# Kernel tuning notes

Measured on AMD Instinct MI355X. Metric: run time of the kernel, lower is better.

The kernel has to match this reference:

```python
import jax, jax.numpy as jnp
import numpy as np


def setup_inputs() -> dict:
    key = jax.random.key(0)
    ks = jax.random.split(key, 8)
    C, G, F = 500, 200, 500          # cells_oi, genes_oi, position bins (fragmentprob_size)
    N_GENES, N_CLUST = 1000, 10      # total genes, clusters
    NFRAG = 5_000_000
    bincounts = jax.random.randint(ks[0], (G, F), 0, 20).astype(jnp.float32)
    baseline_weight = jax.random.normal(ks[1], (N_GENES, F), jnp.float32) * 0.1
    differential_weight = jax.random.normal(ks[2], (N_CLUST, 1, 1), jnp.float32) * 0.01
    cluster_modifier = jax.random.normal(ks[3], (N_CLUST,), jnp.float32) * 0.01
    genes_oi = jax.random.randint(ks[4], (G,), 0, N_GENES)
    labels = jax.random.randint(ks[5], (C,), 0, N_CLUST)
    local_cellxgene_ix = jax.random.randint(ks[6], (NFRAG,), 0, C * G)
    binix = jax.random.randint(ks[7], (NFRAG,), 0, F)
    return dict(bincounts=bincounts, baseline_weight=baseline_weight,
                differential_weight=differential_weight, cluster_modifier=cluster_modifier,
                genes_oi=genes_oi, labels=labels,
                local_cellxgene_ix=local_cellxgene_ix, binix=binix)


def reference(bincounts, baseline_weight, differential_weight, cluster_modifier,
              genes_oi, labels, local_cellxgene_ix, binix):
    G, F = bincounts.shape
    C = labels.shape[0]
    # predictor2 is Identity, final_channels = n_hidden_dims = 1
    gene_embedding = bincounts[:, :, None]                     # [G, F, 1]
    baseline = baseline_weight[genes_oi]                       # [G, F]
    cell_embedding = differential_weight[labels][:, :, 0]      # [C, 1]
    # matmul([1,G,F,H], [C,1,H,1]).squeeze(-1) -> [C,G,F]
    u = (jnp.einsum('gfh,ch->cgf', gene_embedding, cell_embedding)
         + baseline[None]
         + cluster_modifier[labels][:, None, None])            # [C, G, F]
    # histogram of fragments into (cell x gene x bin)
    idx = local_cellxgene_ix * F + binix
    count = jnp.zeros(C * G * F, dtype=u.dtype).at[idx].add(1.0).reshape(C, G, F)
    # Poisson(rate=exp(u)).log_prob(count) = count*u - exp(u) - lgamma(count+1)
    logp = count * u - jnp.exp(u) - jax.lax.lgamma(count + 1.0)
    return logp.sum(-1)                                        # [C, G]
```

## Files before the change

### kernel.cpp

```cpp
#include <hip/hip_runtime.h>
#include <stdint.h>

#define C_   500
#define G_   200
#define F_   500
#define K_   10
#define CG_  (C_ * G_)
#define CGPB 125
#define NBUCK (CG_ / CGPB)
#define NVB  (NBUCK * 2)
#define RSTRIDE 504
#define WPR  (RSTRIDE / 8)
#define NCW2 (CGPB * WPR + 1)
#define TPB_P 1024
#define GRID_P 512
#define NBLK 512
#define TPB_B 512
#define CHUNK_MAX 10240
#define FPT2 (CHUNK_MAX / TPB_P / 2)
#define SLOT 40
#define OVF_CAP 16

__constant__ float LGF[16] = {
    0.0f, 0.0f, 0.69314718f, 1.79175947f, 3.17805383f, 4.78749174f,
    6.57925121f, 8.52516136f, 10.60460290f, 12.80182748f, 15.10441257f,
    17.50230785f, 19.98721450f, 22.55216385f, 25.19122118f, 27.89927138f
};

__global__ __launch_bounds__(TPB_P) void partition_kernel(
        const int* __restrict__ lci,
        const int* __restrict__ binix,
        const float* __restrict__ bc,
        const float* __restrict__ bw,
        const int* __restrict__ genes_oi,
        const float* __restrict__ dw,
        const float* __restrict__ cm,
        uint16_t* __restrict__ frag16,
        uint16_t* __restrict__ cnt16,
        uint32_t* __restrict__ ovfn,
        uint32_t* __restrict__ ovfe,
        float* __restrict__ u_tab,
        float* __restrict__ E,
        int NF, int chunk) {
    __shared__ uint32_t stage[CHUNK_MAX];
    __shared__ uint32_t hist[NVB];
    __shared__ uint32_t vstart[NVB];
    __shared__ uint32_t sstart[NBUCK];
    __shared__ float    psum[4];
    __shared__ uint32_t ovf_lds[OVF_CAP];
    __shared__ uint32_t oc;
    int tid = threadIdx.x;
    int blk = blockIdx.x;
    int copy = tid >> 9;
    int s0 = blk * chunk;
    int s1 = min(s0 + chunk, NF);
    int nloc = s1 - s0;

    for (int b = tid; b < NVB; b += TPB_P) hist[b] = 0;
    if (tid < 4) psum[tid] = 0.0f;
    if (tid == 0) oc = 0u;
    __syncthreads();

    {
        int p = blk * 4 + (tid >> 8);
        if (p < K_ * G_) {
            int sub = tid & 255;
            int k = p / G_;
            int g = p - k * G_;
            float dwk = dw[k];
            float cmk = cm[k];
            const float* bcg = bc + (size_t)g * F_;
            const float* bwg = bw + (size_t)genes_oi[g] * F_;
            float* urow = u_tab + (size_t)p * F_;
            float u0 = dwk * bcg[sub] + bwg[sub] + cmk;
            urow[sub] = u0;
            float s = __expf(u0);
            int f1 = sub + 256;
            if (f1 < F_) {
                float u1 = dwk * bcg[f1] + bwg[f1] + cmk;
                urow[f1] = u1;
                s += __expf(u1);
            }
#pragma unroll
            for (int off = 32; off > 0; off >>= 1) s += __shfl_down(s, off);
            if ((tid & 63) == 0) atomicAdd(&psum[tid >> 8], s);
        }
    }

    uint32_t my_pack[FPT2 * 2], my_rank[FPT2 * 2];
    const int2* lci2 = (const int2*)(lci + s0);
    const int2* bin2 = (const int2*)(binix + s0);
#pragma unroll
    for (int u = 0; u < FPT2; ++u) {
        int pi = u * TPB_P + tid;
        int e0 = pi * 2;
        my_pack[2 * u]     = 0xFFFFFFFFu;
        my_pack[2 * u + 1] = 0xFFFFFFFFu;
        if (e0 + 1 < nloc) {
            int2 cg2 = lci2[pi];
            int2 f2  = bin2[pi];
            uint32_t b0  = (uint32_t)cg2.x / CGPB;
            uint32_t lp0 = ((uint32_t)cg2.x - b0 * CGPB) * RSTRIDE + (uint32_t)f2.x;
            my_pack[2 * u] = (b0 << 16) | lp0;
            my_rank[2 * u] = atomicAdd(&hist[copy * NBUCK + b0], 1u);
            uint32_t b1  = (uint32_t)cg2.y / CGPB;
            uint32_t lp1 = ((uint32_t)cg2.y - b1 * CGPB) * RSTRIDE + (uint32_t)f2.y;
            my_pack[2 * u + 1] = (b1 << 16) | lp1;
            my_rank[2 * u + 1] = atomicAdd(&hist[copy * NBUCK + b1], 1u);
        } else if (e0 < nloc) {
            int cg = lci[s0 + e0];
            int f  = binix[s0 + e0];
            uint32_t b  = (uint32_t)cg / CGPB;
            uint32_t lp = ((uint32_t)cg - b * CGPB) * RSTRIDE + (uint32_t)f;
            my_pack[2 * u] = (b << 16) | lp;
            my_rank[2 * u] = atomicAdd(&hist[copy * NBUCK + b], 1u);
        }
    }
    __syncthreads();

    if (tid < 4) {
        int p = blk * 4 + tid;
        if (p < K_ * G_) E[p] = psum[tid];
    }
    if (tid < 64) {
        int lane = tid;
        uint32_t loc[13];
        uint32_t run = 0;
#pragma unroll
        for (int q = 0; q < 13; ++q) {
            int b = lane * 13 + q;
            uint32_t n = (b < NBUCK) ? (hist[b] + hist[NBUCK + b]) : 0u;
            loc[q] = run;
            run += n;
        }
        uint32_t v = run;
        for (int d = 1; d < 64; d <<= 1) {
            uint32_t t = __shfl_up(v, d);
            if (lane >= d) v += t;
        }
        uint32_t excl = v - run;
#pragma unroll
        for (int q = 0; q < 13; ++q) {
            int b = lane * 13 + q;
            if (b < NBUCK) {
                uint32_t st = excl + loc[q];
                sstart[b] = st;
                vstart[b]         = st;
                vstart[NBUCK + b] = st + hist[b];
            }
        }
    } else if (tid < 64 + NBUCK) {
        int b = tid - 64;
        uint32_t n = hist[b] + hist[NBUCK + b];
        cnt16[(size_t)blk * NBUCK + b] = (uint16_t)min(n, (uint32_t)SLOT);
    }
    __syncthreads();

#pragma unroll
    for (int u = 0; u < FPT2 * 2; ++u) {
        if (my_pack[u] != 0xFFFFFFFFu) {
            uint32_t bb = my_pack[u] >> 16;
            stage[vstart[copy * NBUCK + bb] + my_rank[u]] = my_pack[u];
        }
    }
    __syncthreads();

    for (int j = tid; j < nloc; j += TPB_P) {
        uint32_t v = stage[j];
        uint32_t b = v >> 16;
        uint32_t r = (uint32_t)j - sstart[b];
        if (r < SLOT)
            frag16[((size_t)b * NBLK + blk) * SLOT + r] = (uint16_t)v;
        else {
            uint32_t o = atomicAdd(&oc, 1u);
            if (o < OVF_CAP) ovf_lds[o] = v;
        }
    }
    __syncthreads();
    if (tid == 0) ovfn[blk] = min(oc, (uint32_t)OVF_CAP);
    if (tid < OVF_CAP && tid < oc) ovfe[blk * OVF_CAP + tid] = ovf_lds[tid];
}

__global__ __launch_bounds__(TPB_B) void bucket_kernel(
        const uint16_t* __restrict__ frag16,
        const uint16_t* __restrict__ cnt16,
        const uint32_t* __restrict__ ovfn,
        const uint32_t* __restrict__ ovfe,
        const float* __restrict__ u_tab,
        const float* __restrict__ E,
        const int* __restrict__ labels,
        float* __restrict__ out) {
    __shared__ uint32_t cnt[NCW2];
    __shared__ uint16_t cnts[NBLK];
    __shared__ int pairidx[CGPB];
    int b = blockIdx.x;
    int tid = threadIdx.x;

    uint4* c4 = (uint4*)cnt;
    for (int w = tid; w < NCW2 / 4; w += TPB_B) c4[w] = make_uint4(0u, 0u, 0u, 0u);
    if (tid < CGPB) {
        int cg = b * CGPB + tid;
        int c = cg / G_;
        int g = cg - c * G_;
        pairidx[tid] = labels[c] * G_ + g;
    }
    if (tid < NBLK) cnts[tid] = cnt16[(size_t)tid * NBUCK + b];
    __syncthreads();

    const uint4* fb4 = (const uint4*)(frag16 + (size_t)b * NBLK * SLOT);
    for (int i = tid; i < NBLK * 5; i += TPB_B) {
        uint32_t blk = (uint32_t)i / 5u;
        uint32_t q   = (uint32_t)i - blk * 5u;
        int n  = (int)cnts[blk];
        int j0 = (int)q * 8;
        if (j0 < n) {
            uint4 four = fb4[i];
            int m = n - j0;
            uint32_t w0 = four.x, w1 = four.y, w2 = four.z, w3 = four.w;
            uint32_t wq[4] = {w0, w1, w2, w3};
#pragma unroll
            for (int t = 0; t < 8; ++t) {
                if (t < m) {
                    uint32_t l = (wq[t >> 1] >> ((t & 1) * 16)) & 0xFFFFu;
                    atomicAdd(&cnt[l >> 3], 1u << ((l & 7u) * 4u));
                }
            }
        }
    }
    if (tid < NBLK) {
        uint32_t on = ovfn[tid];
        for (uint32_t q = 0; q < on; ++q) {
            uint32_t e = ovfe[tid * OVF_CAP + q];
            if ((e >> 16) == (uint32_t)b) {
                uint32_t l = e & 0xFFFFu;
                atomicAdd(&cnt[l >> 3], 1u << ((l & 7u) * 4u));
            }
        }
    }
    __syncthreads();

    int wave = tid >> 6, lane = tid & 63;
    for (int r = wave; r < CGPB; r += (TPB_B / 64)) {
        float s = 0.0f;
        if (lane < WPR) {
            uint32_t v = cnt[r * WPR + lane];
            if (v) {
                const float4* up = (const float4*)(u_tab + (size_t)pairidx[r] * F_ + 8 * lane);
                float4 ua = up[0];
                float4 ub = up[1];
                s += (float)( v        & 0xFu) * ua.x
                   + (float)((v >> 4)  & 0xFu) * ua.y
                   + (float)((v >> 8)  & 0xFu) * ua.z
                   + (float)((v >> 12) & 0xFu) * ua.w
                   + (float)((v >> 16) & 0xFu) * ub.x
                   + (float)((v >> 20) & 0xFu) * ub.y
                   + (float)((v >> 24) & 0xFu) * ub.z
                   + (float)((v >> 28)       ) * ub.w;
                if (v & 0xEEEEEEEEu) {
#pragma unroll
                    for (int q = 0; q < 8; ++q)
                        s -= LGF[(v >> (q * 4)) & 0xFu];
                }
            }
        }
#pragma unroll
        for (int off = 32; off > 0; off >>= 1) s += __shfl_down(s, off);
        if (lane == 0) out[b * CGPB + r] = s - E[pairidx[r]];
    }
}

extern "C" void kernel_launch(void* const* d_in, const int* in_sizes, int n_in,
                              void* d_out, int out_size, void* d_ws, size_t ws_size,
                              hipStream_t stream) {
    const float* bc     = (const float*)d_in[0];
    const float* bw     = (const float*)d_in[1];
    const float* dw     = (const float*)d_in[2];
    const float* cm     = (const float*)d_in[3];
    const int* genes_oi = (const int*)d_in[4];
    const int* labels   = (const int*)d_in[5];
    const int* lci      = (const int*)d_in[6];
    const int* binix    = (const int*)d_in[7];
    float* out = (float*)d_out;

    const int NF = in_sizes[6];
    int chunk = (NF + GRID_P - 1) / GRID_P;
    chunk = (chunk + 1) & ~1;
    if (chunk > CHUNK_MAX) chunk = CHUNK_MAX;

    char* ws = (char*)d_ws;
    size_t off_cnt16 = ((size_t)NBUCK * NBLK * SLOT * sizeof(uint16_t) + 255) & ~(size_t)255;
    size_t off_ovfn  = (off_cnt16 + (size_t)NBLK * NBUCK * sizeof(uint16_t) + 255) & ~(size_t)255;
    size_t off_ovfe  = (off_ovfn + NBLK * sizeof(uint32_t) + 255) & ~(size_t)255;
    size_t off_utab  = (off_ovfe + (size_t)NBLK * OVF_CAP * sizeof(uint32_t) + 255) & ~(size_t)255;
    size_t off_E     = (off_utab + ((size_t)K_ * G_ * F_ + 16) * sizeof(float) + 255) & ~(size_t)255;

    uint16_t* frag16 = (uint16_t*)ws;
    uint16_t* cnt16  = (uint16_t*)(ws + off_cnt16);
    uint32_t* ovfn   = (uint32_t*)(ws + off_ovfn);
    uint32_t* ovfe   = (uint32_t*)(ws + off_ovfe);
    float*    u_tab  = (float*)(ws + off_utab);
    float*    E      = (float*)(ws + off_E);

    partition_kernel<<<GRID_P, TPB_P, 0, stream>>>(
        lci, binix, bc, bw, genes_oi, dw, cm,
        frag16, cnt16, ovfn, ovfe, u_tab, E, NF, chunk);

    bucket_kernel<<<NBUCK, TPB_B, 0, stream>>>(
        frag16, cnt16, ovfn, ovfe, u_tab, E, labels, out);
}
```

Baseline: 131.8 us.

## Halve partition block size, double grid, and pack bucket slots into vector stores

Partition now runs 1024 blocks of 512 threads, each with a smaller chunk, so SLOT drops from 40 to 24 and the bucket kernel reads three uint4 per source block instead of five. The scatter into frag16 changes from one 16-bit store per fragment to one thread per bucket that packs eight staged entries into each uint4 store. Occupancy hints are added to both kernels. The cost is a per-bucket serial loop that is less balanced across threads, and with smaller slots more fragments may spill into the overflow path, which is capped at 16 per block.

```diff
diff --git a/kernel.cpp b/kernel.cpp
--- a/kernel.cpp
+++ b/kernel.cpp
@@ -12,13 +12,13 @@
 #define RSTRIDE 504
 #define WPR  (RSTRIDE / 8)
 #define NCW2 (CGPB * WPR + 1)
-#define TPB_P 1024
-#define GRID_P 512
-#define NBLK 512
+#define TPB_P 512
+#define GRID_P 1024
+#define NBLK 1024
 #define TPB_B 512
-#define CHUNK_MAX 10240
-#define FPT2 (CHUNK_MAX / TPB_P / 2)
-#define SLOT 40
+#define CHUNK_MAX 4992
+#define FPT2 5
+#define SLOT 24
 #define OVF_CAP 16
 
 __constant__ float LGF[16] = {
@@ -27,7 +27,7 @@
     17.50230785f, 19.98721450f, 22.55216385f, 25.19122118f, 27.89927138f
 };
 
-__global__ __launch_bounds__(TPB_P) void partition_kernel(
+__global__ __launch_bounds__(TPB_P, 6) void partition_kernel(
         const int* __restrict__ lci,
         const int* __restrict__ binix,
         const float* __restrict__ bc,
@@ -42,27 +42,27 @@
         float* __restrict__ u_tab,
         float* __restrict__ E,
         int NF, int chunk) {
-    __shared__ uint32_t stage[CHUNK_MAX];
+    __shared__ uint32_t stage[CHUNK_MAX + 8];
     __shared__ uint32_t hist[NVB];
     __shared__ uint32_t vstart[NVB];
     __shared__ uint32_t sstart[NBUCK];
-    __shared__ float    psum[4];
+    __shared__ float    psum[2];
     __shared__ uint32_t ovf_lds[OVF_CAP];
     __shared__ uint32_t oc;
     int tid = threadIdx.x;
     int blk = blockIdx.x;
-    int copy = tid >> 9;
+    int copy = tid >> 8;
     int s0 = blk * chunk;
     int s1 = min(s0 + chunk, NF);
     int nloc = s1 - s0;
 
     for (int b = tid; b < NVB; b += TPB_P) hist[b] = 0;
-    if (tid < 4) psum[tid] = 0.0f;
+    if (tid < 2) psum[tid] = 0.0f;
     if (tid == 0) oc = 0u;
     __syncthreads();
 
     {
-        int p = blk * 4 + (tid >> 8);
+        int p = blk * 2 + (tid >> 8);
         if (p < K_ * G_) {
             int sub = tid & 255;
             int k = p / G_;
@@ -118,8 +118,8 @@
     }
     __syncthreads();
 
-    if (tid < 4) {
-        int p = blk * 4 + tid;
+    if (tid < 2) {
+        int p = blk * 2 + tid;
         if (p < K_ * G_) E[p] = psum[tid];
     }
     if (tid < 64) {
@@ -149,10 +149,11 @@
                 vstart[NBUCK + b] = st + hist[b];
             }
         }
-    } else if (tid < 64 + NBUCK) {
-        int b = tid - 64;
-        uint32_t n = hist[b] + hist[NBUCK + b];
-        cnt16[(size_t)blk * NBUCK + b] = (uint16_t)min(n, (uint32_t)SLOT);
+    } else {
+        for (int b = tid - 64; b < NBUCK; b += TPB_P - 64) {
+            uint32_t n = hist[b] + hist[NBUCK + b];
+            cnt16[(size_t)blk * NBUCK + b] = (uint16_t)min(n, (uint32_t)SLOT);
+        }
     }
     __syncthreads();
 
@@ -165,15 +166,33 @@
     }
     __syncthreads();
 
-    for (int j = tid; j < nloc; j += TPB_P) {
-        uint32_t v = stage[j];
-        uint32_t b = v >> 16;
-        uint32_t r = (uint32_t)j - sstart[b];
-        if (r < SLOT)
-            frag16[((size_t)b * NBLK + blk) * SLOT + r] = (uint16_t)v;
-        else {
+    for (int b = tid; b < NBUCK; b += TPB_P) {
+        uint32_t st = sstart[b];
+        uint32_t n  = hist[b] + hist[NBUCK + b];
+        uint32_t nw = min(n, (uint32_t)SLOT);
+        uint4* dst = (uint4*)(frag16 + ((size_t)b * NBLK + blk) * SLOT);
+#pragma unroll
+        for (int q = 0; q < 3; ++q) {
+            if ((uint32_t)(q * 8) < nw) {
+                uint32_t w0 = stage[st + q * 8 + 0];
+                uint32_t w1 = stage[st + q * 8 + 1];
+                uint32_t w2 = stage[st + q * 8 + 2];
+                uint32_t w3 = stage[st + q * 8 + 3];
+                uint32_t w4 = stage[st + q * 8 + 4];
+                uint32_t w5 = stage[st + q * 8 + 5];
+                uint32_t w6 = stage[st + q * 8 + 6];
+                uint32_t w7 = stage[st + q * 8 + 7];
+                uint4 v;
+                v.x = (w0 & 0xFFFFu) | (w1 << 16);
+                v.y = (w2 & 0xFFFFu) | (w3 << 16);
+                v.z = (w4 & 0xFFFFu) | (w5 << 16);
+                v.w = (w6 & 0xFFFFu) | (w7 << 16);
+                dst[q] = v;
+            }
+        }
+        for (uint32_t k = SLOT; k < n; ++k) {
             uint32_t o = atomicAdd(&oc, 1u);
-            if (o < OVF_CAP) ovf_lds[o] = v;
+            if (o < OVF_CAP) ovf_lds[o] = stage[st + k];
         }
     }
     __syncthreads();
@@ -181,7 +200,7 @@
     if (tid < OVF_CAP && tid < oc) ovfe[blk * OVF_CAP + tid] = ovf_lds[tid];
 }
 
-__global__ __launch_bounds__(TPB_B) void bucket_kernel(
+__global__ __launch_bounds__(TPB_B, 8) void bucket_kernel(
         const uint16_t* __restrict__ frag16,
         const uint16_t* __restrict__ cnt16,
         const uint32_t* __restrict__ ovfn,
@@ -204,20 +223,20 @@
         int g = cg - c * G_;
         pairidx[tid] = labels[c] * G_ + g;
     }
-    if (tid < NBLK) cnts[tid] = cnt16[(size_t)tid * NBUCK + b];
+    for (int i = tid; i < NBLK; i += TPB_B)
+        cnts[i] = cnt16[(size_t)i * NBUCK + b];
     __syncthreads();
 
     const uint4* fb4 = (const uint4*)(frag16 + (size_t)b * NBLK * SLOT);
-    for (int i = tid; i < NBLK * 5; i += TPB_B) {
-        uint32_t blk = (uint32_t)i / 5u;
-        uint32_t q   = (uint32_t)i - blk * 5u;
+    for (int i = tid; i < NBLK * 3; i += TPB_B) {
+        uint32_t blk = (uint32_t)i / 3u;
+        uint32_t q   = (uint32_t)i - blk * 3u;
         int n  = (int)cnts[blk];
         int j0 = (int)q * 8;
         if (j0 < n) {
             uint4 four = fb4[i];
             int m = n - j0;
-            uint32_t w0 = four.x, w1 = four.y, w2 = four.z, w3 = four.w;
-            uint32_t wq[4] = {w0, w1, w2, w3};
+            uint32_t wq[4] = {four.x, four.y, four.z, four.w};
 #pragma unroll
             for (int t = 0; t < 8; ++t) {
                 if (t < m) {
@@ -227,10 +246,10 @@
             }
         }
     }
-    if (tid < NBLK) {
-        uint32_t on = ovfn[tid];
+    for (int t = tid; t < NBLK; t += TPB_B) {
+        uint32_t on = ovfn[t];
         for (uint32_t q = 0; q < on; ++q) {
-            uint32_t e = ovfe[tid * OVF_CAP + q];
+            uint32_t e = ovfe[t * OVF_CAP + q];
             if ((e >> 16) == (uint32_t)b) {
                 uint32_t l = e & 0xFFFFu;
                 atomicAdd(&cnt[l >> 3], 1u << ((l & 7u) * 4u));
```

Measured after the change: 137.1 us. 4.0% more time.

## Write fragments directly into fixed per-bucket LDS slots, dropping scan and staging pass

Applied to the files above, without the earlier changes.

The partition kernel no longer builds a two-copy histogram, prefix-scans it, stages packed fragments and then scatters them. Each fragment now takes its rank from a single per-bucket atomic and writes its 16-bit local position straight into a fixed-size per-bucket shared slot array. Whole slots are then copied out with vector stores. SLOT shrinks from 40 to 32 so the bucket kernel reads four 16-byte vectors per source block instead of five, and the overflow capacity grows to cover the tighter slots. This removes a scan, two barriers and the register-held rank arrays, at the cost of more contention on one histogram copy and more overflow-list traffic.

```diff
diff --git a/kernel.cpp b/kernel.cpp
--- a/kernel.cpp
+++ b/kernel.cpp
@@ -8,7 +8,6 @@
 #define CG_  (C_ * G_)
 #define CGPB 125
 #define NBUCK (CG_ / CGPB)
-#define NVB  (NBUCK * 2)
 #define RSTRIDE 504
 #define WPR  (RSTRIDE / 8)
 #define NCW2 (CGPB * WPR + 1)
@@ -18,8 +17,8 @@
 #define TPB_B 512
 #define CHUNK_MAX 10240
 #define FPT2 (CHUNK_MAX / TPB_P / 2)
-#define SLOT 40
-#define OVF_CAP 16
+#define SLOT 32
+#define OVF_CAP 32
 
 __constant__ float LGF[16] = {
     0.0f, 0.0f, 0.69314718f, 1.79175947f, 3.17805383f, 4.78749174f,
@@ -42,21 +41,18 @@
         float* __restrict__ u_tab,
         float* __restrict__ E,
         int NF, int chunk) {
-    __shared__ uint32_t stage[CHUNK_MAX];
-    __shared__ uint32_t hist[NVB];
-    __shared__ uint32_t vstart[NVB];
-    __shared__ uint32_t sstart[NBUCK];
+    __shared__ uint16_t smem16[NBUCK * SLOT];
+    __shared__ uint32_t hist[NBUCK];
     __shared__ float    psum[4];
     __shared__ uint32_t ovf_lds[OVF_CAP];
     __shared__ uint32_t oc;
     int tid = threadIdx.x;
     int blk = blockIdx.x;
-    int copy = tid >> 9;
     int s0 = blk * chunk;
     int s1 = min(s0 + chunk, NF);
     int nloc = s1 - s0;
 
-    for (int b = tid; b < NVB; b += TPB_P) hist[b] = 0;
+    if (tid < NBUCK) hist[tid] = 0;
     if (tid < 4) psum[tid] = 0.0f;
     if (tid == 0) oc = 0u;
     __syncthreads();
@@ -87,33 +83,46 @@
         }
     }
 
-    uint32_t my_pack[FPT2 * 2], my_rank[FPT2 * 2];
     const int2* lci2 = (const int2*)(lci + s0);
     const int2* bin2 = (const int2*)(binix + s0);
 #pragma unroll
     for (int u = 0; u < FPT2; ++u) {
         int pi = u * TPB_P + tid;
         int e0 = pi * 2;
-        my_pack[2 * u]     = 0xFFFFFFFFu;
-        my_pack[2 * u + 1] = 0xFFFFFFFFu;
         if (e0 + 1 < nloc) {
             int2 cg2 = lci2[pi];
             int2 f2  = bin2[pi];
-            uint32_t b0  = (uint32_t)cg2.x / CGPB;
-            uint32_t lp0 = ((uint32_t)cg2.x - b0 * CGPB) * RSTRIDE + (uint32_t)f2.x;
-            my_pack[2 * u] = (b0 << 16) | lp0;
-            my_rank[2 * u] = atomicAdd(&hist[copy * NBUCK + b0], 1u);
-            uint32_t b1  = (uint32_t)cg2.y / CGPB;
-            uint32_t lp1 = ((uint32_t)cg2.y - b1 * CGPB) * RSTRIDE + (uint32_t)f2.y;
-            my_pack[2 * u + 1] = (b1 << 16) | lp1;
-            my_rank[2 * u + 1] = atomicAdd(&hist[copy * NBUCK + b1], 1u);
+            {
+                uint32_t b  = (uint32_t)cg2.x / CGPB;
+                uint32_t lp = ((uint32_t)cg2.x - b * CGPB) * RSTRIDE + (uint32_t)f2.x;
+                uint32_t r  = atomicAdd(&hist[b], 1u);
+                if (r < SLOT) smem16[b * SLOT + r] = (uint16_t)lp;
+                else {
+                    uint32_t o = atomicAdd(&oc, 1u);
+                    if (o < OVF_CAP) ovf_lds[o] = (b << 16) | lp;
+                }
+            }
+            {
+                uint32_t b  = (uint32_t)cg2.y / CGPB;
+                uint32_t lp = ((uint32_t)cg2.y - b * CGPB) * RSTRIDE + (uint32_t)f2.y;
+                uint32_t r  = atomicAdd(&hist[b], 1u);
+                if (r < SLOT) smem16[b * SLOT + r] = (uint16_t)lp;
+                else {
+                    uint32_t o = atomicAdd(&oc, 1u);
+                    if (o < OVF_CAP) ovf_lds[o] = (b << 16) | lp;
+                }
+            }
         } else if (e0 < nloc) {
             int cg = lci[s0 + e0];
             int f  = binix[s0 + e0];
             uint32_t b  = (uint32_t)cg / CGPB;
             uint32_t lp = ((uint32_t)cg - b * CGPB) * RSTRIDE + (uint32_t)f;
-            my_pack[2 * u] = (b << 16) | lp;
-            my_rank[2 * u] = atomicAdd(&hist[copy * NBUCK + b], 1u);
+            uint32_t r  = atomicAdd(&hist[b], 1u);
+            if (r < SLOT) smem16[b * SLOT + r] = (uint16_t)lp;
+            else {
+                uint32_t o = atomicAdd(&oc, 1u);
+                if (o < OVF_CAP) ovf_lds[o] = (b << 16) | lp;
+            }
         }
     }
     __syncthreads();
@@ -122,61 +131,20 @@
         int p = blk * 4 + tid;
         if (p < K_ * G_) E[p] = psum[tid];
     }
-    if (tid < 64) {
-        int lane = tid;
-        uint32_t loc[13];
-        uint32_t run = 0;
-#pragma unroll
-        for (int q = 0; q < 13; ++q) {
-            int b = lane * 13 + q;
-            uint32_t n = (b < NBUCK) ? (hist[b] + hist[NBUCK + b]) : 0u;
-            loc[q] = run;
-            run += n;
-        }
-        uint32_t v = run;
-        for (int d = 1; d < 64; d <<= 1) {
-            uint32_t t = __shfl_up(v, d);
-            if (lane >= d) v += t;
-        }
-        uint32_t excl = v - run;
-#pragma unroll
-        for (int q = 0; q < 13; ++q) {
-            int b = lane * 13 + q;
-            if (b < NBUCK) {
-                uint32_t st = excl + loc[q];
-                sstart[b] = st;
-                vstart[b]         = st;
-                vstart[NBUCK + b] = st + hist[b];
-            }
-        }
-    } else if (tid < 64 + NBUCK) {
-        int b = tid - 64;
-        uint32_t n = hist[b] + hist[NBUCK + b];
-        cnt16[(size_t)blk * NBUCK + b] = (uint16_t)min(n, (uint32_t)SLOT);
-    }
-    __syncthreads();
-
-#pragma unroll
-    for (int u = 0; u < FPT2 * 2; ++u) {
-        if (my_pack[u] != 0xFFFFFFFFu) {
-            uint32_t bb = my_pack[u] >> 16;
-            stage[vstart[copy * NBUCK + bb] + my_rank[u]] = my_pack[u];
-        }
-    }
-    __syncthreads();
-
-    for (int j = tid; j < nloc; j += TPB_P) {
-        uint32_t v = stage[j];
-        uint32_t b = v >> 16;
-        uint32_t r = (uint32_t)j - sstart[b];
-        if (r < SLOT)
-            frag16[((size_t)b * NBLK + blk) * SLOT + r] = (uint16_t)v;
-        else {
-            uint32_t o = atomicAdd(&oc, 1u);
-            if (o < OVF_CAP) ovf_lds[o] = v;
-        }
-    }
-    __syncthreads();
+    if (tid < NBUCK)
+        cnt16[(size_t)blk * NBUCK + tid] = (uint16_t)min(hist[tid], (uint32_t)SLOT);
+
+    const uint4* s4 = (const uint4*)smem16;
+    for (int i = tid; i < NBUCK * 4; i += TPB_P) {
+        int seg = i >> 2;
+        int q   = i & 3;
+        uint32_t n = min(hist[seg], (uint32_t)SLOT);
+        if ((uint32_t)(q * 8) < n) {
+            uint4* dst = (uint4*)(frag16 + ((size_t)seg * NBLK + blk) * SLOT);
+            dst[q] = s4[i];
+        }
+    }
+
     if (tid == 0) ovfn[blk] = min(oc, (uint32_t)OVF_CAP);
     if (tid < OVF_CAP && tid < oc) ovfe[blk * OVF_CAP + tid] = ovf_lds[tid];
 }
@@ -208,16 +176,15 @@
     __syncthreads();
 
     const uint4* fb4 = (const uint4*)(frag16 + (size_t)b * NBLK * SLOT);
-    for (int i = tid; i < NBLK * 5; i += TPB_B) {
-        uint32_t blk = (uint32_t)i / 5u;
-        uint32_t q   = (uint32_t)i - blk * 5u;
-        int n  = (int)cnts[blk];
+    for (int i = tid; i < NBLK * 4; i += TPB_B) {
+        uint32_t blkq = (uint32_t)i >> 2;
+        uint32_t q    = (uint32_t)i & 3u;
+        int n  = (int)cnts[blkq];
         int j0 = (int)q * 8;
         if (j0 < n) {
             uint4 four = fb4[i];
             int m = n - j0;
-            uint32_t w0 = four.x, w1 = four.y, w2 = four.z, w3 = four.w;
-            uint32_t wq[4] = {w0, w1, w2, w3};
+            uint32_t wq[4] = {four.x, four.y, four.z, four.w};
 #pragma unroll
             for (int t = 0; t < 8; ++t) {
                 if (t < m) {
```

After: 126.3 us. -4.2%, faster.
